# Kernel optimization log

Hardware: AMD Instinct MI355X
Metric: run time of the kernel (lower is better)

Reference implementation:

```python
import jax, jax.numpy as jnp
import numpy as np

NEG_SLOPE = 0.01  # PyTorch LeakyReLU default

def lrelu(x):
    return jnp.where(x >= 0, x, NEG_SLOPE * x)

def setup_inputs() -> dict:
    key = jax.random.key(0)
    ks = jax.random.split(key, 16)
    d, nu, ni, nr = 64, 50000, 25000, 400000
    s = 1.0 / np.sqrt(d)
    f = jnp.float32
    return {
        "Xu": jax.random.normal(ks[0], (nu, d), f),
        "Xi": jax.random.normal(ks[1], (ni, d), f),
        "Wsrc": jax.random.normal(ks[2], (d, d), f) * s,
        "bsrc": jnp.zeros((d,), f),
        "Wdst": jax.random.normal(ks[3], (d, d), f) * s,
        "bdst": jnp.zeros((d,), f),
        "watt_rep": jax.random.normal(ks[4], (d,), f) * s,
        "batt_rep": jnp.zeros((), f),
        "Wo": jax.random.normal(ks[5], (d, d), f) * s,
        "bo": jnp.zeros((d,), f),
        "Wu": jax.random.normal(ks[6], (d, d), f) * s,
        "bu": jnp.zeros((d,), f),
        "watt_agg": jax.random.normal(ks[7], (d,), f) * s,
        "batt_agg": jnp.zeros((), f),
        "pref_user": jax.random.normal(ks[8], (nu, d), f),
        "pref_item": jax.random.normal(ks[9], (ni, d), f),
        "r_user": jax.random.randint(ks[10], (400000,), 0, nu),
        "r_item": jax.random.randint(ks[11], (400000,), 0, ni),
    }

def reference(Xu, Xi, Wsrc, bsrc, Wdst, bdst, watt_rep, batt_rep,
              Wo, bo, Wu, bu, watt_agg, batt_agg,
              pref_user, pref_item, r_user, r_item):
    nu, ni = Xu.shape[0], Xi.shape[0]
    # ---- ReviewRepresentationConv ----
    # Each review has exactly one user edge and one item edge, so per-etype
    # mean over edges is a gather; cross-type 'mean' averages the two types.
    agg = 0.5 * (Xu[r_user] + Xi[r_item])                 # [R, d]
    hs_u = Xu @ Wsrc + bsrc                               # src_w_a(x)
    hs_i = Xi @ Wsrc + bsrc
    hd_r = agg @ Wdst + bdst                              # dst_w_a(agg)
    # raw exp attention (module uses torch.exp, not stable edge_softmax here)
    a_u = jnp.exp(lrelu(hs_u[r_user] + hd_r) @ watt_rep + batt_rep)  # [R]
    a_i = jnp.exp(lrelu(hs_i[r_item] + hd_r) @ watt_rep + batt_rep)
    denom = a_u + a_i                                     # e_div_v normalizer
    h_rev = (a_u / denom)[:, None] * Xu[r_user] + (a_i / denom)[:, None] * Xi[r_item]
    # ---- ReviewAggregatorConv ----
    h_o = h_rev @ Wo + bo                                 # w_o(src review feats)

    def agg_side(npid_emb, dst, n_dst):
        z = lrelu(h_o + npid_emb @ Wu + bu)               # u_add_e then LeakyReLU
        a = z @ watt_agg + batt_agg                       # [R] attention logits
        m = jax.ops.segment_max(a, dst, num_segments=n_dst)
        e = jnp.exp(a - m[dst])                           # stable edge_softmax
        ssum = jax.ops.segment_sum(e, dst, num_segments=n_dst)
        w = e / ssum[dst]
        # u_mul_e + sum scatter-reduce
        return jax.ops.segment_sum(h_rev * w[:, None], dst, num_segments=n_dst)

    out_user = agg_side(pref_item[r_item], r_user, nu)    # [nu, d]
    out_item = agg_side(pref_user[r_user], r_item, ni)    # [ni, d]
    return jnp.concatenate([out_user, out_item], axis=0)  # [nu+ni, d]
```

## Files before the change

### kernel.cpp

```cpp
#include <hip/hip_runtime.h>
#include <hip/hip_fp16.h>
#include <math.h>

#define D 64
#define EPB 1024

typedef _Float16 f16x8 __attribute__((ext_vector_type(8)));
typedef _Float16 f16x4 __attribute__((ext_vector_type(4)));
typedef float f32x4 __attribute__((ext_vector_type(4)));

__device__ __forceinline__ float lrelu(float x) { return fmaxf(x, 0.f) + 0.01f * fminf(x, 0.f); }

__global__ void k_init(int4* __restrict__ p, int n4) {
    int i = blockIdx.x * blockDim.x + threadIdx.x;
    int stride = gridDim.x * blockDim.x;
    int4 z = make_int4(0, 0, 0, 0);
    for (int j = i; j < n4; j += stride) p[j] = z;
}

__global__ void k_count(const int* __restrict__ ru, const int* __restrict__ ri,
                        int* __restrict__ cnt_u, int* __restrict__ cnt_i, int R) {
    int r = blockIdx.x * blockDim.x + threadIdx.x;
    if (r >= R) return;
    atomicAdd(&cnt_u[ru[r]], 1);
    atomicAdd(&cnt_i[ri[r]], 1);
}

__global__ void k_fill_u(const int* __restrict__ ru, const int* __restrict__ ri,
                         int* __restrict__ cur_u, int2* __restrict__ edges, int R) {
    int r = blockIdx.x * blockDim.x + threadIdx.x;
    if (r >= R) return;
    int u = ru[r], it = ri[r];
    int j = atomicAdd(&cur_u[u], 1);
    edges[j] = make_int2(u, it);
}

__global__ __launch_bounds__(256) void k_nodes_mfma(
    const float* __restrict__ Xu, const float* __restrict__ Pu, int nu, int ntu,
    const float* __restrict__ Xi_, const float* __restrict__ Pi, int ni, int nti,
    const float* __restrict__ Wsrc, const float* __restrict__ bsrc,
    const float* __restrict__ Wdst, const float* __restrict__ bdst,
    const float* __restrict__ Wo,   const float* __restrict__ bo,
    const float* __restrict__ Wu,   const float* __restrict__ bu,
    __half* __restrict__ packU, __half* __restrict__ Xuh,
    __half* __restrict__ packI, __half* __restrict__ Xih) {
    __shared__ float sX[16 * 68];
    __shared__ float sP[16 * 68];
    __shared__ __half sD[4][16][72];
    __shared__ float sb[4][64];
    int tid = threadIdx.x;
    int lane = tid & 63, w = tid >> 6;
    int col = lane & 15, kg = lane >> 4;

    {
        int c = tid & 63, m = tid >> 6;
        const float* bp = (m == 0) ? bsrc : (m == 1) ? bdst : (m == 2) ? bo : bu;
        sb[m][c] = bp[c];
    }
    const float* W = (w == 0) ? Wsrc : (w == 1) ? Wdst : (w == 2) ? Wo : Wu;
    f16x8 Bf[2][4];
#pragma unroll
    for (int kt = 0; kt < 2; ++kt)
#pragma unroll
        for (int ct = 0; ct < 4; ++ct) {
            int c = ct * 16 + col;
            int k0 = kt * 32 + kg * 8;
            f16x8 bfrag;
#pragma unroll
            for (int j = 0; j < 8; ++j) bfrag[j] = (_Float16)W[(k0 + j) * 64 + c];
            Bf[kt][ct] = bfrag;
        }
    __syncthreads();

    int T = ntu + nti;
    for (int tile = blockIdx.x; tile < T; tile += gridDim.x) {
        bool usr = tile < ntu;
        const float* X = usr ? Xu : Xi_;
        const float* P = usr ? Pu : Pi;
        __half* pack = usr ? packU : packI;
        __half* Xh = usr ? Xuh : Xih;
        int n = usr ? nu : ni;
        int nb = (usr ? tile : tile - ntu) * 16;

        {
            int rl = tid >> 4;
            int c0s = (tid & 15) * 4;
            int grow = nb + rl; if (grow >= n) grow = n - 1;
            *(float4*)&sX[rl * 68 + c0s] = *(const float4*)(X + (size_t)grow * 64 + c0s);
            *(float4*)&sP[rl * 68 + c0s] = *(const float4*)(P + (size_t)grow * 64 + c0s);
        }
        __syncthreads();
        const float* srow = (w == 3) ? &sP[col * 68] : &sX[col * 68];
        float4 a0 = *(const float4*)(srow + kg * 8);
        float4 a1 = *(const float4*)(srow + kg * 8 + 4);
        float4 a2 = *(const float4*)(srow + 32 + kg * 8);
        float4 a3 = *(const float4*)(srow + 32 + kg * 8 + 4);
        f16x8 A0, A1;
        A0[0] = (_Float16)a0.x; A0[1] = (_Float16)a0.y; A0[2] = (_Float16)a0.z; A0[3] = (_Float16)a0.w;
        A0[4] = (_Float16)a1.x; A0[5] = (_Float16)a1.y; A0[6] = (_Float16)a1.z; A0[7] = (_Float16)a1.w;
        A1[0] = (_Float16)a2.x; A1[1] = (_Float16)a2.y; A1[2] = (_Float16)a2.z; A1[3] = (_Float16)a2.w;
        A1[4] = (_Float16)a3.x; A1[5] = (_Float16)a3.y; A1[6] = (_Float16)a3.z; A1[7] = (_Float16)a3.w;
        if (w == 0) {
            int arow = nb + col; if (arow >= n) arow = n - 1;
            *(f16x8*)(Xh + (size_t)arow * 64 + kg * 8) = A0;
            *(f16x8*)(Xh + (size_t)arow * 64 + 32 + kg * 8) = A1;
        }
        f32x4 acc[4];
#pragma unroll
        for (int ct = 0; ct < 4; ++ct) {
            acc[ct] = (f32x4){0.f, 0.f, 0.f, 0.f};
            acc[ct] = __builtin_amdgcn_mfma_f32_16x16x32_f16(A0, Bf[0][ct], acc[ct], 0, 0, 0);
            acc[ct] = __builtin_amdgcn_mfma_f32_16x16x32_f16(A1, Bf[1][ct], acc[ct], 0, 0, 0);
        }
        __syncthreads();
#pragma unroll
        for (int ct = 0; ct < 4; ++ct)
#pragma unroll
            for (int jj = 0; jj < 4; ++jj)
                sD[w][kg * 4 + jj][ct * 16 + col] = __float2half(acc[ct][jj]);
        __syncthreads();
        int r = tid >> 4, c0 = (tid & 15) * 4;
        int node = nb + r;
        if (node < n) {
            __half* dst = pack + (size_t)node * 256;
            f16x4 v[4];
#pragma unroll
            for (int q = 0; q < 4; ++q) {
                int c = c0 + q;
                float hs = __half2float(sD[0][r][c]) + sb[0][c];
                float hds = 0.5f * (__half2float(sD[1][r][c]) + sb[1][c]);
                float ho = __half2float(sD[2][r][c]) + sb[2][c];
                float pw = __half2float(sD[3][r][c]) + sb[3][c];
                v[0][q] = (_Float16)(hs + hds);
                v[1][q] = (_Float16)hds;
                v[2][q] = (_Float16)ho;
                v[3][q] = (_Float16)pw;
            }
#pragma unroll
            for (int m = 0; m < 4; ++m)
                *(f16x4*)(dst + m * 64 + c0) = v[m];
        }
    }
}

__global__ __launch_bounds__(256, 1) void k_rev1(
    const int2* __restrict__ edges,
    const __half* __restrict__ packU, const __half* __restrict__ packI,
    const float4* __restrict__ watt_rep4,
    const float4* __restrict__ watt_agg4, const float* __restrict__ batt_agg,
    int* __restrict__ cur_i,
    float4* __restrict__ pay_su, float4* __restrict__ pay_si,
    int R) {
    int tid = threadIdx.x;
    int lane = tid & 63;
    int f = lane & 7;
    int j = blockIdx.x * 32 + (tid >> 6) * 8 + (lane >> 3);
    if (j >= R) return;
    int2 e = edges[j];
    const __half* pu = packU + (size_t)e.x * 256 + f * 8;
    const __half* pi = packI + (size_t)e.y * 256 + f * 8;
    f16x8 f0u = *(const f16x8*)(pu);
    f16x8 hdu = *(const f16x8*)(pu + 64);
    f16x8 hou = *(const f16x8*)(pu + 128);
    f16x8 pwu = *(const f16x8*)(pu + 192);
    f16x8 f0i = *(const f16x8*)(pi);
    f16x8 hdi = *(const f16x8*)(pi + 64);
    f16x8 hoi = *(const f16x8*)(pi + 128);
    f16x8 pwi = *(const f16x8*)(pi + 192);

    f16x8 xu = f0u + hdi;
    f16x8 xi = f0i + hdu;
    float4 wrA = watt_rep4[f * 2], wrB = watt_rep4[f * 2 + 1];
    float tu =
        lrelu((float)xu[0]) * wrA.x + lrelu((float)xu[1]) * wrA.y +
        lrelu((float)xu[2]) * wrA.z + lrelu((float)xu[3]) * wrA.w +
        lrelu((float)xu[4]) * wrB.x + lrelu((float)xu[5]) * wrB.y +
        lrelu((float)xu[6]) * wrB.z + lrelu((float)xu[7]) * wrB.w;
    float ti =
        lrelu((float)xi[0]) * wrA.x + lrelu((float)xi[1]) * wrA.y +
        lrelu((float)xi[2]) * wrA.z + lrelu((float)xi[3]) * wrA.w +
        lrelu((float)xi[4]) * wrB.x + lrelu((float)xi[5]) * wrB.y +
        lrelu((float)xi[6]) * wrB.z + lrelu((float)xi[7]) * wrB.w;
#pragma unroll
    for (int o = 4; o; o >>= 1) {
        tu += __shfl_xor(tu, o, 64);
        ti += __shfl_xor(ti, o, 64);
    }
    float wu = 1.f / (1.f + __expf(ti - tu));
    float wi = 1.f - wu;
    float4 waA = watt_agg4[f * 2], waB = watt_agg4[f * 2 + 1];
    float zu = 0.f, zi = 0.f;
#pragma unroll
    for (int k = 0; k < 8; ++k) {
        float ho = wu * (float)hou[k] + wi * (float)hoi[k];
        float wa = (k < 4) ? ((const float*)&waA)[k] : ((const float*)&waB)[k - 4];
        zu += lrelu(ho + (float)pwi[k]) * wa;
        zi += lrelu(ho + (float)pwu[k]) * wa;
    }
#pragma unroll
    for (int o = 4; o; o >>= 1) {
        zu += __shfl_xor(zu, o, 64);
        zi += __shfl_xor(zi, o, 64);
    }
    if (f == 0) {
        float ba = batt_agg[0];
        pay_su[j] = make_float4(zu + ba, wu, __int_as_float(e.y), 0.f);
        int j2 = atomicAdd(&cur_i[e.y], 1);
        pay_si[j2] = make_float4(zi + ba, wu, __int_as_float(e.x), 0.f);
    }
}

__global__ __launch_bounds__(256) void k_scan_local(
    const int* __restrict__ cnt_u, int* __restrict__ off_u, int nu,
    const int* __restrict__ cnt_i, int* __restrict__ off_i, int ni,
    int* __restrict__ bsum, int Bu) {
    int b = blockIdx.x;
    const int* cnt; int* off; int n; int lb;
    if (b < Bu) { cnt = cnt_u; off = off_u; n = nu; lb = b; }
    else        { cnt = cnt_i; off = off_i; n = ni; lb = b - Bu; }
    int t = threadIdx.x;
    int idx0 = lb * EPB + t * 4;
    int v[4];
#pragma unroll
    for (int k = 0; k < 4; ++k) v[k] = (idx0 + k < n) ? cnt[idx0 + k] : 0;
    int s = v[0] + v[1] + v[2] + v[3];
    int lane = t & 63, w = t >> 6;
    int x = s;
#pragma unroll
    for (int o = 1; o < 64; o <<= 1) {
        int y = __shfl_up(x, o, 64);
        if (lane >= o) x += y;
    }
    __shared__ int wsum[4];
    if (lane == 63) wsum[w] = x;
    __syncthreads();
    int woff = 0;
    for (int j = 0; j < w; ++j) woff += wsum[j];
    int run = woff + x - s;
#pragma unroll
    for (int k = 0; k < 4; ++k) {
        if (idx0 + k < n) off[idx0 + k] = run;
        run += v[k];
    }
    if (t == 255) bsum[b] = woff + x;
}

__global__ __launch_bounds__(256) void k_scan_add(
    int* __restrict__ off_u, int* __restrict__ cur_u, int nu,
    int* __restrict__ off_i, int* __restrict__ cur_i, int ni,
    const int* __restrict__ bsum, int Bu, int Bi) {
    int b = blockIdx.x;
    int* off; int* cur; int n; int lb; const int* bs; int B;
    if (b < Bu) { off = off_u; cur = cur_u; n = nu; lb = b; bs = bsum; B = Bu; }
    else        { off = off_i; cur = cur_i; n = ni; lb = b - Bu; bs = bsum + Bu; B = Bi; }
    int boff = 0;
    for (int j = 0; j < lb; ++j) boff += bs[j];
    int idx0 = lb * EPB + threadIdx.x * 4;
#pragma unroll
    for (int k = 0; k < 4; ++k) {
        int idx = idx0 + k;
        if (idx < n) {
            int vv = off[idx] + boff;
            off[idx] = vv;
            cur[idx] = vv;
        }
    }
    if (lb == B - 1 && threadIdx.x == 0) off[n] = boff + bs[lb];
}

__global__ __launch_bounds__(256, 1) void k_agg(
    const int* __restrict__ off_u, const int* __restrict__ off_i,
    const float4* __restrict__ pay_su, const float4* __restrict__ pay_si,
    const float* __restrict__ Xu, const float* __restrict__ Xi,
    const __half* __restrict__ Xuh, const __half* __restrict__ Xih,
    float* __restrict__ out, int nu, int ntot) {
    int tid = threadIdx.x;
    int lane = tid & 63;
    int idx = blockIdx.x * 4 + (tid >> 6);
    if (idx >= ntot) return;
    bool user = idx < nu;
    int d = user ? idx : idx - nu;
    const int*    offp = user ? off_u : off_i;
    const float4* pay  = user ? pay_su : pay_si;
    const float*  Xown = user ? Xu : Xi;
    const __half* Xoth = user ? Xih : Xuh;
    int s = offp[d], e = offp[d + 1];
    if (s == e) { out[(size_t)idx * D + lane] = 0.f; return; }
    int g = lane >> 3;
    int l = lane & 7;
    float msum = 0.f, mcoef = 0.f;
    float acc[8] = {0.f, 0.f, 0.f, 0.f, 0.f, 0.f, 0.f, 0.f};
    for (int j = s + g; j < e; j += 8) {
        float4 p = pay[j];
        float ex = __expf(p.x);
        float wown = user ? p.y : 1.f - p.y;
        msum += ex;
        mcoef += ex * wown;
        float cv = ex * (1.f - wown);
        int o2 = __float_as_int(p.z);
        const __half2* row = (const __half2*)(Xoth + (size_t)o2 * D + 8 * l);
        float2 f0 = __half22float2(row[0]);
        float2 f1 = __half22float2(row[1]);
        float2 f2 = __half22float2(row[2]);
        float2 f3 = __half22float2(row[3]);
        acc[0] += cv * f0.x; acc[1] += cv * f0.y;
        acc[2] += cv * f1.x; acc[3] += cv * f1.y;
        acc[4] += cv * f2.x; acc[5] += cv * f2.y;
        acc[6] += cv * f3.x; acc[7] += cv * f3.y;
    }
#pragma unroll
    for (int o = 32; o >= 8; o >>= 1) {
        msum  += __shfl_xor(msum, o, 64);
        mcoef += __shfl_xor(mcoef, o, 64);
#pragma unroll
        for (int q = 0; q < 8; ++q) acc[q] += __shfl_xor(acc[q], o, 64);
    }
    if (g == 0) {
        float inv = 1.f / msum;
        const float4* xo = (const float4*)(Xown + (size_t)d * D + 8 * l);
        float4 x0 = xo[0], x1 = xo[1];
        float4 r0, r1;
        r0.x = (mcoef * x0.x + acc[0]) * inv;
        r0.y = (mcoef * x0.y + acc[1]) * inv;
        r0.z = (mcoef * x0.z + acc[2]) * inv;
        r0.w = (mcoef * x0.w + acc[3]) * inv;
        r1.x = (mcoef * x1.x + acc[4]) * inv;
        r1.y = (mcoef * x1.y + acc[5]) * inv;
        r1.z = (mcoef * x1.z + acc[6]) * inv;
        r1.w = (mcoef * x1.w + acc[7]) * inv;
        float4* op = (float4*)(out + (size_t)idx * D + 8 * l);
        op[0] = r0;
        op[1] = r1;
    }
}

extern "C" void kernel_launch(void* const* d_in, const int* in_sizes, int n_in,
                              void* d_out, int out_size, void* d_ws, size_t ws_size,
                              hipStream_t stream) {
    const float* Xu        = (const float*)d_in[0];
    const float* Xi        = (const float*)d_in[1];
    const float* Wsrc      = (const float*)d_in[2];
    const float* bsrc      = (const float*)d_in[3];
    const float* Wdst      = (const float*)d_in[4];
    const float* bdst      = (const float*)d_in[5];
    const float* watt_rep  = (const float*)d_in[6];
    const float* batt_rep  = (const float*)d_in[7];  (void)batt_rep;
    const float* Wo        = (const float*)d_in[8];
    const float* bo        = (const float*)d_in[9];
    const float* Wu        = (const float*)d_in[10];
    const float* bu        = (const float*)d_in[11];
    const float* watt_agg  = (const float*)d_in[12];
    const float* batt_agg  = (const float*)d_in[13];
    const float* pref_user = (const float*)d_in[14];
    const float* pref_item = (const float*)d_in[15];
    const int* r_user      = (const int*)d_in[16];
    const int* r_item      = (const int*)d_in[17];

    int nu = in_sizes[0] / D;
    int ni = in_sizes[1] / D;
    int R  = in_sizes[16];

    float* ws = (float*)d_ws;
    size_t off = 0;
    __half* packU = (__half*)(ws + off); off += (size_t)nu * D * 2;
    __half* packI = (__half*)(ws + off); off += (size_t)ni * D * 2;
    __half* Xuh = (__half*)(ws + off); off += (size_t)nu * D / 2;
    __half* Xih = (__half*)(ws + off); off += (size_t)ni * D / 2;
    float4* pay_su = (float4*)(ws + off); off += (size_t)R * 4;
    float4* pay_si = (float4*)(ws + off); off += (size_t)R * 4;
    int2* edges = (int2*)(ws + off); off += (size_t)R * 2;
    int* cnt_u = (int*)(ws + off); off += (size_t)nu;
    int* cnt_i = (int*)(ws + off); off += (size_t)ni;
    int* bsum  = (int*)(ws + off); off += 256;
    int* off_u = (int*)(ws + off); off += (size_t)nu + 1;
    int* off_i = (int*)(ws + off); off += (size_t)ni + 1;

    int n4 = (nu + ni + 3) / 4;
    k_init<<<128, 256, 0, stream>>>((int4*)cnt_u, n4);

    k_count<<<(R + 255) / 256, 256, 0, stream>>>(r_user, r_item, cnt_u, cnt_i, R);

    int Bu = (nu + EPB - 1) / EPB, Bi = (ni + EPB - 1) / EPB;
    k_scan_local<<<Bu + Bi, 256, 0, stream>>>(
        cnt_u, off_u, nu, cnt_i, off_i, ni, bsum, Bu);
    k_scan_add<<<Bu + Bi, 256, 0, stream>>>(
        off_u, cnt_u, nu, off_i, cnt_i, ni, bsum, Bu, Bi);

    k_fill_u<<<(R + 255) / 256, 256, 0, stream>>>(r_user, r_item, cnt_u, edges, R);

    int ntu = (nu + 15) / 16, nti = (ni + 15) / 16;
    k_nodes_mfma<<<1024, 256, 0, stream>>>(
        Xu, pref_user, nu, ntu, Xi, pref_item, ni, nti,
        Wsrc, bsrc, Wdst, bdst, Wo, bo, Wu, bu,
        packU, Xuh, packI, Xih);

    k_rev1<<<(R + 31) / 32, 256, 0, stream>>>(
        edges, packU, packI,
        (const float4*)watt_rep, (const float4*)watt_agg, batt_agg,
        cnt_i, pay_su, pay_si, R);

    int ntot = nu + ni;
    k_agg<<<(ntot + 3) / 4, 256, 0, stream>>>(
        off_u, off_i, pay_su, pay_si,
        Xu, Xi, Xuh, Xih, (float*)d_out, nu, ntot);
}
```

Baseline: 164.6 us.

## Fold counter zeroing into node GEMM and merge scan into single-pass decoupled scan

Removes the separate zero-init kernel by having the node MFMA kernel clear the count and flag arrays. It also replaces the two-kernel block scan with one kernel that publishes block sums through release/acquire flags and spin-waits on earlier blocks. This cuts two kernel launches and one pass over the offsets array. In exchange it relies on forward progress of earlier-indexed blocks for the spin-wait, and the scan kernel reads and writes cnt through aliased pointers marked restrict.

```diff
diff --git a/kernel.cpp b/kernel.cpp
--- a/kernel.cpp
+++ b/kernel.cpp
@@ -10,13 +10,6 @@
 typedef float f32x4 __attribute__((ext_vector_type(4)));
 
 __device__ __forceinline__ float lrelu(float x) { return fmaxf(x, 0.f) + 0.01f * fminf(x, 0.f); }
-
-__global__ void k_init(int4* __restrict__ p, int n4) {
-    int i = blockIdx.x * blockDim.x + threadIdx.x;
-    int stride = gridDim.x * blockDim.x;
-    int4 z = make_int4(0, 0, 0, 0);
-    for (int j = i; j < n4; j += stride) p[j] = z;
-}
 
 __global__ void k_count(const int* __restrict__ ru, const int* __restrict__ ri,
                         int* __restrict__ cnt_u, int* __restrict__ cnt_i, int R) {
@@ -43,7 +36,8 @@
     const float* __restrict__ Wo,   const float* __restrict__ bo,
     const float* __restrict__ Wu,   const float* __restrict__ bu,
     __half* __restrict__ packU, __half* __restrict__ Xuh,
-    __half* __restrict__ packI, __half* __restrict__ Xih) {
+    __half* __restrict__ packI, __half* __restrict__ Xih,
+    int* __restrict__ zero_region, int nzero) {
     __shared__ float sX[16 * 68];
     __shared__ float sP[16 * 68];
     __shared__ __half sD[4][16][72];
@@ -51,6 +45,9 @@
     int tid = threadIdx.x;
     int lane = tid & 63, w = tid >> 6;
     int col = lane & 15, kg = lane >> 4;
+
+    for (int j = blockIdx.x * 256 + tid; j < nzero; j += gridDim.x * 256)
+        zero_region[j] = 0;
 
     {
         int c = tid & 63, m = tid >> 6;
@@ -141,6 +138,62 @@
                 *(f16x4*)(dst + m * 64 + c0) = v[m];
         }
     }
+}
+
+__global__ __launch_bounds__(256) void k_scan1(
+    const int* __restrict__ cnt_u, int* __restrict__ off_u, int* __restrict__ cur_u, int nu,
+    const int* __restrict__ cnt_i, int* __restrict__ off_i, int* __restrict__ cur_i, int ni,
+    int* __restrict__ bsum, int* __restrict__ flags, int Bu, int Bi) {
+    int b = blockIdx.x;
+    const int* cnt; int* off; int* cur; int n; int lb; int sb_; int B;
+    if (b < Bu) { cnt = cnt_u; off = off_u; cur = cur_u; n = nu; lb = b; sb_ = 0;  B = Bu; }
+    else        { cnt = cnt_i; off = off_i; cur = cur_i; n = ni; lb = b - Bu; sb_ = Bu; B = Bi; }
+    int t = threadIdx.x;
+    int idx0 = lb * EPB + t * 4;
+    int v[4];
+#pragma unroll
+    for (int k = 0; k < 4; ++k) v[k] = (idx0 + k < n) ? cnt[idx0 + k] : 0;
+    int s = v[0] + v[1] + v[2] + v[3];
+    int lane = t & 63, w = t >> 6;
+    int x = s;
+#pragma unroll
+    for (int o = 1; o < 64; o <<= 1) {
+        int y = __shfl_up(x, o, 64);
+        if (lane >= o) x += y;
+    }
+    __shared__ int wsum[4];
+    __shared__ int sboff;
+    if (lane == 63) wsum[w] = x;
+    __syncthreads();
+    int woff = 0;
+    for (int j = 0; j < w; ++j) woff += wsum[j];
+    int run = woff + x - s;
+    int tot = wsum[0] + wsum[1] + wsum[2] + wsum[3];
+    if (t == 0) {
+        bsum[b] = tot;
+        __threadfence();
+        __hip_atomic_store(&flags[b], 1, __ATOMIC_RELEASE, __HIP_MEMORY_SCOPE_AGENT);
+        int boff = 0;
+        for (int j = sb_; j < b; ++j) {
+            while (__hip_atomic_load(&flags[j], __ATOMIC_ACQUIRE,
+                                     __HIP_MEMORY_SCOPE_AGENT) == 0) { }
+            boff += bsum[j];
+        }
+        sboff = boff;
+    }
+    __syncthreads();
+    int boff = sboff;
+#pragma unroll
+    for (int k = 0; k < 4; ++k) {
+        int idx = idx0 + k;
+        if (idx < n) {
+            int vv = run + boff;
+            off[idx] = vv;
+            cur[idx] = vv;
+        }
+        run += v[k];
+    }
+    if (lb == B - 1 && t == 0) off[n] = boff + tot;
 }
 
 __global__ __launch_bounds__(256, 1) void k_rev1(
@@ -208,64 +261,6 @@
         int j2 = atomicAdd(&cur_i[e.y], 1);
         pay_si[j2] = make_float4(zi + ba, wu, __int_as_float(e.x), 0.f);
     }
-}
-
-__global__ __launch_bounds__(256) void k_scan_local(
-    const int* __restrict__ cnt_u, int* __restrict__ off_u, int nu,
-    const int* __restrict__ cnt_i, int* __restrict__ off_i, int ni,
-    int* __restrict__ bsum, int Bu) {
-    int b = blockIdx.x;
-    const int* cnt; int* off; int n; int lb;
-    if (b < Bu) { cnt = cnt_u; off = off_u; n = nu; lb = b; }
-    else        { cnt = cnt_i; off = off_i; n = ni; lb = b - Bu; }
-    int t = threadIdx.x;
-    int idx0 = lb * EPB + t * 4;
-    int v[4];
-#pragma unroll
-    for (int k = 0; k < 4; ++k) v[k] = (idx0 + k < n) ? cnt[idx0 + k] : 0;
-    int s = v[0] + v[1] + v[2] + v[3];
-    int lane = t & 63, w = t >> 6;
-    int x = s;
-#pragma unroll
-    for (int o = 1; o < 64; o <<= 1) {
-        int y = __shfl_up(x, o, 64);
-        if (lane >= o) x += y;
-    }
-    __shared__ int wsum[4];
-    if (lane == 63) wsum[w] = x;
-    __syncthreads();
-    int woff = 0;
-    for (int j = 0; j < w; ++j) woff += wsum[j];
-    int run = woff + x - s;
-#pragma unroll
-    for (int k = 0; k < 4; ++k) {
-        if (idx0 + k < n) off[idx0 + k] = run;
-        run += v[k];
-    }
-    if (t == 255) bsum[b] = woff + x;
-}
-
-__global__ __launch_bounds__(256) void k_scan_add(
-    int* __restrict__ off_u, int* __restrict__ cur_u, int nu,
-    int* __restrict__ off_i, int* __restrict__ cur_i, int ni,
-    const int* __restrict__ bsum, int Bu, int Bi) {
-    int b = blockIdx.x;
-    int* off; int* cur; int n; int lb; const int* bs; int B;
-    if (b < Bu) { off = off_u; cur = cur_u; n = nu; lb = b; bs = bsum; B = Bu; }
-    else        { off = off_i; cur = cur_i; n = ni; lb = b - Bu; bs = bsum + Bu; B = Bi; }
-    int boff = 0;
-    for (int j = 0; j < lb; ++j) boff += bs[j];
-    int idx0 = lb * EPB + threadIdx.x * 4;
-#pragma unroll
-    for (int k = 0; k < 4; ++k) {
-        int idx = idx0 + k;
-        if (idx < n) {
-            int vv = off[idx] + boff;
-            off[idx] = vv;
-            cur[idx] = vv;
-        }
-    }
-    if (lb == B - 1 && threadIdx.x == 0) off[n] = boff + bs[lb];
 }
 
 __global__ __launch_bounds__(256, 1) void k_agg(
@@ -371,28 +366,25 @@
     int2* edges = (int2*)(ws + off); off += (size_t)R * 2;
     int* cnt_u = (int*)(ws + off); off += (size_t)nu;
     int* cnt_i = (int*)(ws + off); off += (size_t)ni;
-    int* bsum  = (int*)(ws + off); off += 256;
+    int* flags = (int*)(ws + off); off += 128;
+    int* bsum  = (int*)(ws + off); off += 128;
     int* off_u = (int*)(ws + off); off += (size_t)nu + 1;
     int* off_i = (int*)(ws + off); off += (size_t)ni + 1;
 
-    int n4 = (nu + ni + 3) / 4;
-    k_init<<<128, 256, 0, stream>>>((int4*)cnt_u, n4);
-
-    k_count<<<(R + 255) / 256, 256, 0, stream>>>(r_user, r_item, cnt_u, cnt_i, R);
-
-    int Bu = (nu + EPB - 1) / EPB, Bi = (ni + EPB - 1) / EPB;
-    k_scan_local<<<Bu + Bi, 256, 0, stream>>>(
-        cnt_u, off_u, nu, cnt_i, off_i, ni, bsum, Bu);
-    k_scan_add<<<Bu + Bi, 256, 0, stream>>>(
-        off_u, cnt_u, nu, off_i, cnt_i, ni, bsum, Bu, Bi);
-
-    k_fill_u<<<(R + 255) / 256, 256, 0, stream>>>(r_user, r_item, cnt_u, edges, R);
-
+    int nzero = nu + ni + 128;
     int ntu = (nu + 15) / 16, nti = (ni + 15) / 16;
     k_nodes_mfma<<<1024, 256, 0, stream>>>(
         Xu, pref_user, nu, ntu, Xi, pref_item, ni, nti,
         Wsrc, bsrc, Wdst, bdst, Wo, bo, Wu, bu,
-        packU, Xuh, packI, Xih);
+        packU, Xuh, packI, Xih, cnt_u, nzero);
+
+    k_count<<<(R + 255) / 256, 256, 0, stream>>>(r_user, r_item, cnt_u, cnt_i, R);
+
+    int Bu = (nu + EPB - 1) / EPB, Bi = (ni + EPB - 1) / EPB;
+    k_scan1<<<Bu + Bi, 256, 0, stream>>>(
+        cnt_u, off_u, cnt_u, nu, cnt_i, off_i, cnt_i, ni, bsum, flags, Bu, Bi);
+
+    k_fill_u<<<(R + 255) / 256, 256, 0, stream>>>(r_user, r_item, cnt_u, edges, R);
 
     k_rev1<<<(R + 31) / 32, 256, 0, stream>>>(
         edges, packU, packI,
```

Result: slower. 177.4 us (+7.8%).
